# Kernel optimization log

Hardware: AMD Instinct MI355X
Metric: run time of the kernel (lower is better)

## Reference

```python
import jax, jax.numpy as jnp
import numpy as np

IN_F, OUT_F, NB = 4096, 4096, 8
BS = IN_F // NB  # 512


def setup_inputs() -> dict:
    key = jax.random.key(0)
    k1, k2, k3, k4 = jax.random.split(key, 4)
    weight = jax.random.normal(k1, (OUT_F, IN_F), dtype=jnp.float32) * 0.02
    bias = jax.random.normal(k2, (OUT_F,), dtype=jnp.float32) * 0.02
    x = jax.random.normal(k3, (4, 2048, IN_F), dtype=jnp.float32)
    R_blocks = jax.random.normal(k4, (NB, BS, BS), dtype=jnp.float32) * 0.1
    return {"weight": weight, "bias": bias, "x": x, "R_blocks": R_blocks, "layer_idx": 0}


def cayley_transform(A):
    # A: [nb, bs, bs]; Q = (I - A_skew) @ inv(I + A_skew + 1e-6 I)
    bs = A.shape[-1]
    I = jnp.eye(bs, dtype=A.dtype)
    A_skew = 0.5 * (A - jnp.swapaxes(A, -2, -1))
    return jnp.matmul(I - A_skew, jnp.linalg.inv(I + A_skew + 1e-6 * I))


def reference(weight, bias, x, R_blocks, layer_idx):
    R_ortho = cayley_transform(R_blocks)  # [nb, bs, bs]
    # weight @ block_diag(R) == per-block contraction on the in_features axis
    w = weight.reshape(OUT_F, NB, BS)
    tw = jnp.einsum('onb,nbc->onc', w, R_ortho).reshape(OUT_F, IN_F)
    # F.linear: x @ tw.T + bias
    out = jnp.einsum('bsi,oi->bso', x, tw) + bias
    return out
```

## Files before the change

### kernel.cpp

```cpp
#include <hip/hip_runtime.h>
#include <hip/hip_bf16.h>


typedef unsigned short u16;
typedef __attribute__((ext_vector_type(8))) __bf16 bf16x8;
typedef __attribute__((ext_vector_type(4))) float f32x4;
typedef __attribute__((ext_vector_type(8))) unsigned short u16x8;
typedef __attribute__((ext_vector_type(4))) unsigned short u16x4;

#define C0   1.000001f
#define C1Q  2.000001f
#define AS1 __attribute__((address_space(1)))
#define AS3 __attribute__((address_space(3)))

__device__ __forceinline__ u16 f2bf(float x) {
  union { float f; unsigned u; } v; v.f = x;
  return (u16)((v.u + 0x7fffu + ((v.u >> 16) & 1u)) >> 16);
}
__device__ __forceinline__ float bf2f(u16 h) {
  union { float f; unsigned u; } v; v.u = ((unsigned)h) << 16; return v.f;
}

__global__ __launch_bounds__(256) void k_build_M(const float* __restrict__ R,
                                                 u16* __restrict__ Mh,
                                                 u16* __restrict__ Ml) {
  __shared__ float t1[32][33];
  const int n = blockIdx.z;
  const int tr = blockIdx.y * 32, tc = blockIdx.x * 32;
  const int ly = threadIdx.x >> 5, lx = threadIdx.x & 31;
  const float* Rb = R + (size_t)n * 262144;
  float a[4];
#pragma unroll
  for (int i = 0; i < 4; ++i) {
    a[i] = Rb[(size_t)(tr + ly + i * 8) * 512 + tc + lx];
    t1[ly + i * 8][lx] = Rb[(size_t)(tc + ly + i * 8) * 512 + tr + lx];
  }
  __syncthreads();
#pragma unroll
  for (int i = 0; i < 4; ++i) {
    const int r = tr + ly + i * 8, c = tc + lx;
    float m = 0.5f * (a[i] - t1[lx][ly + i * 8]) + (r == c ? C0 : 0.0f);
    u16 h = f2bf(m);
    const size_t idx = (size_t)n * 262144 + (size_t)r * 512 + c;
    Mh[idx] = h;
    Ml[idx] = f2bf(m - bf2f(h));
  }
}

__global__ __launch_bounds__(1024) void k_frob_alpha(const u16* __restrict__ G4,
                                                     float* __restrict__ alpha) {
  __shared__ float red[16];
  const int n = blockIdx.x, tid = threadIdx.x;
  const u16* src = G4 + (size_t)n * 262144;
  float s = 0.f;
  for (int i = tid; i < 32768; i += 1024) {
    u16x8 v = reinterpret_cast<const u16x8*>(src)[i];
#pragma unroll
    for (int e = 0; e < 8; ++e) { float f = bf2f(v[e]); s += f * f; }
  }
  for (int off = 32; off; off >>= 1) s += __shfl_down(s, off, 64);
  if ((tid & 63) == 0) red[tid >> 6] = s;
  __syncthreads();
  if (tid == 0) {
    float t = 0.f;
    for (int q = 0; q < 16; ++q) t += red[q];
    float lam = powf(t, 0.125f);
    alpha[n] = 2.0f / (C0 * C0 + lam);
  }
}

__global__ __launch_bounds__(256) void k_init_X0(const u16* __restrict__ Mh,
                                                 const u16* __restrict__ Ml,
                                                 const float* __restrict__ alpha,
                                                 u16* __restrict__ X0,
                                                 u16* __restrict__ X0t) {
  int idx = blockIdx.x * 256 + threadIdx.x;
  int n = idx >> 18, r = (idx >> 9) & 511, c = idx & 511;
  float m = bf2f(Mh[idx]) + bf2f(Ml[idx]);
  float a = alpha[n];
  X0[idx]  = f2bf(a * ((r == c ? 2.0f * C0 : 0.0f) - m));
  X0t[idx] = f2bf(a * m);
}

template <int PROD3, int DMODE, int OMODE>
__global__ __launch_bounds__(256)
void k_bmm(const u16* __restrict__ Ah, const u16* __restrict__ Al,
           const u16* __restrict__ Bh, const u16* __restrict__ Bl,
           const u16* __restrict__ Dh, const u16* __restrict__ Dl,
           u16* __restrict__ Cnh, u16* __restrict__ Cnl,
           u16* __restrict__ Cth, u16* __restrict__ Ctl,
           float* __restrict__ Cf, float cd, float cs) {
  __shared__ __align__(16) u16 sAh[2048], sBh[2048];
  __shared__ __align__(16) u16 sAl[PROD3 ? 2048 : 8], sBl[PROD3 ? 2048 : 8];
  const size_t zb = (size_t)blockIdx.z * 262144;
  const int tid = threadIdx.x, lane = tid & 63, wave = tid >> 6;
  const int m0 = blockIdx.y * 64, n0 = blockIdx.x * 64;
  const int wr = wave >> 1, wc = wave & 1;
  const int c15 = lane & 15, lk = lane >> 4;
  const int srow = tid >> 2;
  const int sg = (tid & 3) ^ (srow & 3);
  f32x4 acc[2][2] = {};
  const u16* pa = Ah + zb + (size_t)(m0 + srow) * 512 + sg * 8;
  const u16* pb = Bh + zb + (size_t)(n0 + srow) * 512 + sg * 8;

  for (int k0 = 0; k0 < 512; k0 += 32) {
    __builtin_amdgcn_global_load_lds((const AS1 void*)(pa + k0),
                                     (AS3 void*)(sAh + (size_t)tid * 8), 16, 0, 0);
    __builtin_amdgcn_global_load_lds((const AS1 void*)(pb + k0),
                                     (AS3 void*)(sBh + (size_t)tid * 8), 16, 0, 0);
    if constexpr (PROD3) {
      const u16* pal = Al + zb + (size_t)(m0 + srow) * 512 + sg * 8;
      const u16* pbl = Bl + zb + (size_t)(n0 + srow) * 512 + sg * 8;
      __builtin_amdgcn_global_load_lds((const AS1 void*)(pal + k0),
                                       (AS3 void*)(sAl + (size_t)tid * 8), 16, 0, 0);
      __builtin_amdgcn_global_load_lds((const AS1 void*)(pbl + k0),
                                       (AS3 void*)(sBl + (size_t)tid * 8), 16, 0, 0);
    }
    __syncthreads();
    bf16x8 a[2], b[2], al2[2], bl2[2];
#pragma unroll
    for (int i = 0; i < 2; ++i) {
      const int fr = wr * 32 + i * 16 + c15;
      const int ia = fr * 32 + ((lk ^ (fr & 3)) * 8);
      a[i] = *reinterpret_cast<const bf16x8*>(&sAh[ia]);
      if constexpr (PROD3) al2[i] = *reinterpret_cast<const bf16x8*>(&sAl[ia]);
    }
#pragma unroll
    for (int j = 0; j < 2; ++j) {
      const int fc = wc * 32 + j * 16 + c15;
      const int ib = fc * 32 + ((lk ^ (fc & 3)) * 8);
      b[j] = *reinterpret_cast<const bf16x8*>(&sBh[ib]);
      if constexpr (PROD3) bl2[j] = *reinterpret_cast<const bf16x8*>(&sBl[ib]);
    }
#pragma unroll
    for (int i = 0; i < 2; ++i)
#pragma unroll
      for (int j = 0; j < 2; ++j) {
        acc[i][j] = __builtin_amdgcn_mfma_f32_16x16x32_bf16(a[i], b[j], acc[i][j], 0, 0, 0);
        if constexpr (PROD3) {
          acc[i][j] = __builtin_amdgcn_mfma_f32_16x16x32_bf16(a[i],   bl2[j], acc[i][j], 0, 0, 0);
          acc[i][j] = __builtin_amdgcn_mfma_f32_16x16x32_bf16(al2[i], b[j],   acc[i][j], 0, 0, 0);
        }
      }
    __syncthreads();
  }
#pragma unroll
  for (int i = 0; i < 2; ++i)
#pragma unroll
    for (int j = 0; j < 2; ++j) {
      const int rowb = m0 + wr * 32 + i * 16 + lk * 4;
      const int col  = n0 + wc * 32 + j * 16 + c15;
      u16 hv[4], lv[4];
#pragma unroll
      for (int r = 0; r < 4; ++r) {
        float val = cs * acc[i][j][r];
        if constexpr (DMODE >= 1) {
          float d = bf2f(Dh[zb + (size_t)(rowb + r) * 512 + col]);
          if constexpr (DMODE == 2) d += bf2f(Dl[zb + (size_t)(rowb + r) * 512 + col]);
          val += cd * d;
        }
        if constexpr (OMODE & 16) Cf[zb + (size_t)(rowb + r) * 512 + col] = val;
        u16 h = f2bf(val);
        if constexpr (OMODE & 1) Cnh[zb + (size_t)(rowb + r) * 512 + col] = h;
        u16 l = 0;
        if constexpr (OMODE & 10) l = f2bf(val - bf2f(h));
        if constexpr (OMODE & 2) Cnl[zb + (size_t)(rowb + r) * 512 + col] = l;
        hv[r] = h; lv[r] = l;
      }
      if constexpr (OMODE & 4) {
        u16x4 v; v[0] = hv[0]; v[1] = hv[1]; v[2] = hv[2]; v[3] = hv[3];
        *reinterpret_cast<u16x4*>(&Cth[zb + (size_t)col * 512 + rowb]) = v;
      }
      if constexpr (OMODE & 8) {
        u16x4 v; v[0] = lv[0]; v[1] = lv[1]; v[2] = lv[2]; v[3] = lv[3];
        *reinterpret_cast<u16x4*>(&Ctl[zb + (size_t)col * 512 + rowb]) = v;
      }
    }
}

template <int SPLIT, int BF16OUT>
__global__ __launch_bounds__(256)
void k_smm(const float* __restrict__ A, int lda, long long astride,
           const float* __restrict__ B, int ldb, long long bstride,
           void* __restrict__ Cv, int ldc, long long cstride,
           const float* __restrict__ D, int ldd, long long dstride,
           float c1, float sgn, int K) {
  __shared__ __align__(16) u16 lA  [128 * 40];
  __shared__ __align__(16) u16 lBT [128 * 40];
  const int nz = blockIdx.z;
  const float* Ab = A + (size_t)nz * astride;
  const float* Bb = B + (size_t)nz * bstride;
  const float* Db = D + (size_t)nz * dstride;
  const int tid = threadIdx.x, lane = tid & 63, wave = tid >> 6;
  const int m0 = blockIdx.y * 128, n0 = blockIdx.x * 128;
  const int wr = wave >> 1, wc = wave & 1;
  f32x4 acc[4][4] = {};

  for (int k0 = 0; k0 < K; k0 += 32) {
    if (k0) __syncthreads();
    {
      const int row = tid >> 1, ks = (tid & 1) * 16;
      const float* src = Ab + (size_t)(m0 + row) * lda + k0 + ks;
      float fv[16];
#pragma unroll
      for (int q = 0; q < 4; ++q) {
        float4 f = *(reinterpret_cast<const float4*>(src) + q);
        fv[q * 4 + 0] = f.x; fv[q * 4 + 1] = f.y; fv[q * 4 + 2] = f.z; fv[q * 4 + 3] = f.w;
      }
      u16x8 w0, w1;
#pragma unroll
      for (int e = 0; e < 8; ++e) { w0[e] = f2bf(fv[e]); w1[e] = f2bf(fv[e + 8]); }
      *reinterpret_cast<u16x8*>(&lA[row * 40 + ks])     = w0;
      *reinterpret_cast<u16x8*>(&lA[row * 40 + ks + 8]) = w1;
    }
    {
      const int kk = tid >> 3, nb = (tid & 7) * 16;
      const float* src = Bb + (size_t)(k0 + kk) * ldb + n0 + nb;
      float fv[16];
#pragma unroll
      for (int q = 0; q < 4; ++q) {
        float4 f = *(reinterpret_cast<const float4*>(src) + q);
        fv[q * 4 + 0] = f.x; fv[q * 4 + 1] = f.y; fv[q * 4 + 2] = f.z; fv[q * 4 + 3] = f.w;
      }
#pragma unroll
      for (int e = 0; e < 16; ++e) lBT[(nb + e) * 40 + kk] = f2bf(fv[e]);
    }
    __syncthreads();
    const int ks = (lane >> 4) * 8;
    bf16x8 af[4], bfr[4];
#pragma unroll
    for (int f = 0; f < 4; ++f) {
      const int ar = wr * 64 + f * 16 + (lane & 15);
      const int bc = wc * 64 + f * 16 + (lane & 15);
      af[f]  = *reinterpret_cast<const bf16x8*>(&lA [ar * 40 + ks]);
      bfr[f] = *reinterpret_cast<const bf16x8*>(&lBT[bc * 40 + ks]);
    }
#pragma unroll
    for (int i = 0; i < 4; ++i)
#pragma unroll
      for (int j = 0; j < 4; ++j)
        acc[i][j] = __builtin_amdgcn_mfma_f32_16x16x32_bf16(af[i], bfr[j], acc[i][j], 0, 0, 0);
  }
#pragma unroll
  for (int i = 0; i < 4; ++i) {
    const int rowb = m0 + wr * 64 + i * 16 + ((lane >> 4) << 2);
#pragma unroll
    for (int j = 0; j < 4; ++j) {
      const int col = n0 + wc * 64 + j * 16 + (lane & 15);
#pragma unroll
      for (int r = 0; r < 4; ++r) {
        float val = sgn * acc[i][j][r];
        if (c1 != 0.0f) val += c1 * Db[(size_t)(rowb + r) * ldd + col];
        if constexpr (BF16OUT)
          reinterpret_cast<u16*>(Cv)[(size_t)nz * cstride + (size_t)(rowb + r) * ldc + col] = f2bf(val);
        else
          reinterpret_cast<float*>(Cv)[(size_t)nz * cstride + (size_t)(rowb + r) * ldc + col] = val;
      }
    }
  }
}

__global__ __launch_bounds__(256) void k_f32_to_bf16(const float* __restrict__ in,
                                                     u16* __restrict__ out) {
  int idx = blockIdx.x * 256 + threadIdx.x;
  const float* src = in + (size_t)idx * 8;
  float4 f0 = *reinterpret_cast<const float4*>(src);
  float4 f1 = *reinterpret_cast<const float4*>(src + 4);
  u16x8 w;
  w[0] = f2bf(f0.x); w[1] = f2bf(f0.y); w[2] = f2bf(f0.z); w[3] = f2bf(f0.w);
  w[4] = f2bf(f1.x); w[5] = f2bf(f1.y); w[6] = f2bf(f1.z); w[7] = f2bf(f1.w);
  *reinterpret_cast<u16x8*>(out + (size_t)idx * 8) = w;
}

#define NSLOT 9

#define PHASE(KH, MH, WM)                                                      \
  {                                                                            \
    const int gsk = gs0 ^ ((KH) ? 4 : 0);                                      \
    if ((MH) == 0) {                                                           \
      _Pragma("unroll")                                                        \
      for (int n = 0; n < 4; ++n)                                              \
        bf[n] = *reinterpret_cast<const bf16x8*>(                              \
            &lds[bslot * 8192 + (bro + n * 16) * 64 + gsk * 8]);               \
    }                                                                          \
    _Pragma("unroll")                                                          \
    for (int m = 0; m < 4; ++m)                                                \
      af[m] = *reinterpret_cast<const bf16x8*>(                                \
          &lds[aslot * 8192 + ((MH) * 64 + m * 16 + c15) * 64 + gsk * 8]);     \
    STAGE();                                                                   \
    __builtin_amdgcn_s_barrier();                                              \
    asm volatile("s_waitcnt lgkmcnt(0)" ::: "memory");                         \
    __builtin_amdgcn_sched_barrier(0);                                         \
    __builtin_amdgcn_s_setprio(1);                                             \
    _Pragma("unroll")                                                          \
    for (int m = 0; m < 4; ++m)                                                \
      _Pragma("unroll")                                                        \
      for (int n = 0; n < 4; ++n)                                              \
        acc[(MH) * 4 + m][n] = __builtin_amdgcn_mfma_f32_16x16x32_bf16(        \
            af[m], bf[n], acc[(MH) * 4 + m][n], 0, 0, 0);                      \
    __builtin_amdgcn_s_setprio(0);                                             \
    __builtin_amdgcn_sched_barrier(0);                                         \
    if ((WM) == 1) asm volatile("s_waitcnt vmcnt(2)" ::: "memory");            \
    if ((WM) == 2) asm volatile("s_waitcnt vmcnt(0)" ::: "memory");            \
    __builtin_amdgcn_s_barrier();                                              \
  }

#define ADV()                                                                  \
  aslot += 4; if (aslot >= NSLOT) aslot -= NSLOT;                              \
  bslot += 4; if (bslot >= NSLOT) bslot -= NSLOT;

__global__ __launch_bounds__(512, 2)
void k_gemm256(const u16* __restrict__ A, const u16* __restrict__ B,
               const float* __restrict__ bias,
               float* __restrict__ C, int N, int K) {
  __shared__ __align__(16) u16 lds[NSLOT * 8192];
  const int tid = threadIdx.x, lane = tid & 63, wave = tid >> 6;
  int bid = blockIdx.y * gridDim.x + blockIdx.x;
  const int cpx = (gridDim.x * gridDim.y) >> 3;
  bid = (bid & 7) * cpx + (bid >> 3);
  const int nbx = N >> 8;
  const int bx = bid % nbx, by = bid / nbx;
  const int m0 = by << 8, n0 = bx << 8;
  const int wr = wave >> 2, wc = wave & 3;
  const int srow = tid >> 3;
  const int scg  = (tid & 7) ^ (srow & 7);
  const int c15 = lane & 15, lq = lane >> 4;
  const int gs0 = lq ^ (lane & 7);
  const int bro = (wc & 1) * 64 + c15;
  const int NT = K >> 6;

  f32x4 acc[8][4] = {};
  bf16x8 af[4], bf[4];

  int jn = 0, jslot = 0;
  auto STAGE = [&]() {
    if (jn < 4 * NT) {
      const int tau_s = jn >> 2, qh = jn & 3;
      const u16* srcb = (qh < 2)
          ? A + (size_t)(m0 + (qh & 1) * 128 + srow) * (size_t)K
          : B + (size_t)(n0 + (qh & 1) * 128 + srow) * (size_t)K;
      const u16* src = srcb + (tau_s << 6) + scg * 8;
      u16* dst = (u16*)lds + jslot * 8192 + wave * 512;
      __builtin_amdgcn_global_load_lds(
          (const AS1 void*)src, (AS3 void*)dst, 16, 0, 0);
      __builtin_amdgcn_global_load_lds(
          (const AS1 void*)(src + (size_t)64 * K), (AS3 void*)(dst + 4096), 16, 0, 0);
    }
    ++jn; jslot = (jslot == NSLOT - 1) ? 0 : jslot + 1;
  };

  STAGE(); STAGE(); STAGE(); STAGE(); STAGE();
  asm volatile("s_waitcnt vmcnt(2)" ::: "memory");
  __builtin_amdgcn_sched_barrier(0);
  __builtin_amdgcn_s_barrier();

  int aslot = wr, bslot = 2 + (wc >> 1);
  for (int tau = 0; tau < NT - 2; ++tau) {
    PHASE(0, 0, 0)
    PHASE(0, 1, 0)
    PHASE(1, 0, 0)
    PHASE(1, 1, 1)
    ADV()
  }
  PHASE(0, 0, 0)
  PHASE(0, 1, 0)
  PHASE(1, 0, 0)
  PHASE(1, 1, 2)
  ADV()
  PHASE(0, 0, 0)
  PHASE(0, 1, 0)
  PHASE(1, 0, 0)
  PHASE(1, 1, 0)

#pragma unroll
  for (int n = 0; n < 4; ++n) {
    const int col = n0 + wc * 64 + n * 16 + c15;
    const float bv = bias[col];
#pragma unroll
    for (int mi = 0; mi < 8; ++mi) {
      const int rowb = m0 + wr * 128 + mi * 16 + (lq << 2);
#pragma unroll
      for (int r = 0; r < 4; ++r)
        C[(size_t)(rowb + r) * N + col] = acc[mi][n][r] + bv;
    }
  }
}

extern "C" void kernel_launch(void* const* d_in, const int* in_sizes, int n_in,
                              void* d_out, int out_size, void* d_ws, size_t ws_size,
                              hipStream_t stream) {
  const float* W    = (const float*)d_in[0];
  const float* bias = (const float*)d_in[1];
  const float* x    = (const float*)d_in[2];
  const float* R    = (const float*)d_in[3];
  float* out = (float*)d_out;

  char* ws = (char*)d_ws;
  u16* x_bf = (u16*)(ws);
  u16* tw   = (u16*)(ws + 67108864);

  char* arena = (char*)d_out;
  auto slot = [&](int i) -> u16* { return (u16*)(arena + (size_t)i * 4194304); };
  u16 *Mh = slot(0), *Ml = slot(1);
  u16 *G = slot(2), *G2 = slot(3), *G4 = slot(4);
  u16 *Xa = slot(5), *Xat = slot(6), *Xb = slot(7), *Xbt = slot(8);
  u16 *Xbl = slot(9), *Xbtl = slot(10);
  u16 *Tt = slot(2);
  u16 *Tth = slot(3), *Ttl = slot(4);
  u16 *X6h = slot(5), *X6l = slot(6);
  u16 *X6th = slot(11), *X6tl = slot(12);
  float* Qf = (float*)(arena + (size_t)13 * 4194304);
  float* alpha = (float*)(arena + (size_t)15 * 4194304);

  const long long BS2 = 262144;
  const dim3 g8(8, 8, 8);
  const u16* NUL = nullptr;

  k_build_M<<<dim3(16, 16, 8), 256, 0, stream>>>(R, Mh, Ml);
  k_bmm<0, 0, 1><<<g8, 256, 0, stream>>>(Mh, NUL, Mh, NUL, NUL, NUL,
                                         G, nullptr, nullptr, nullptr, nullptr, 0.f, 1.f);
  k_bmm<0, 0, 1><<<g8, 256, 0, stream>>>(G, NUL, G, NUL, NUL, NUL,
                                         G2, nullptr, nullptr, nullptr, nullptr, 0.f, 1.f);
  k_bmm<0, 0, 1><<<g8, 256, 0, stream>>>(G2, NUL, G2, NUL, NUL, NUL,
                                         G4, nullptr, nullptr, nullptr, nullptr, 0.f, 1.f);
  k_frob_alpha<<<8, 1024, 0, stream>>>(G4, alpha);
  k_init_X0<<<8192, 256, 0, stream>>>(Mh, Ml, alpha, Xa, Xat);

  u16 *cur = Xa, *curt = Xat, *nxt = Xb, *nxtt = Xbt;
  for (int it = 0; it < 4; ++it) {
    k_bmm<0, 0, 4><<<g8, 256, 0, stream>>>(Mh, NUL, curt, NUL, NUL, NUL,
                                           nullptr, nullptr, Tt, nullptr, nullptr, 0.f, 1.f);
    k_bmm<0, 1, 5><<<g8, 256, 0, stream>>>(cur, NUL, Tt, NUL, cur, NUL,
                                           nxt, nullptr, nxtt, nullptr, nullptr, 2.f, -1.f);
    u16* t;
    t = cur; cur = nxt; nxt = t;
    t = curt; curt = nxtt; nxtt = t;
  }
  k_bmm<0, 0, 4><<<g8, 256, 0, stream>>>(Mh, NUL, curt, NUL, NUL, NUL,
                                         nullptr, nullptr, Tt, nullptr, nullptr, 0.f, 1.f);
  k_bmm<0, 1, 15><<<g8, 256, 0, stream>>>(cur, NUL, Tt, NUL, cur, NUL,
                                          Xb, Xbl, Xbt, Xbtl, nullptr, 2.f, -1.f);
  k_bmm<1, 0, 12><<<g8, 256, 0, stream>>>(Mh, Ml, Xbt, Xbtl, NUL, NUL,
                                          nullptr, nullptr, Tth, Ttl, nullptr, 0.f, 1.f);
  k_bmm<1, 2, 15><<<g8, 256, 0, stream>>>(Xb, Xbl, Tth, Ttl, Xb, Xbl,
                                          X6h, X6l, X6th, X6tl, nullptr, 2.f, -1.f);
  k_bmm<1, 2, 16><<<g8, 256, 0, stream>>>(Mh, Ml, X6th, X6tl, X6h, X6l,
                                          nullptr, nullptr, nullptr, nullptr, Qf, C1Q, -1.f);
  k_smm<0, 1><<<dim3(4, 32, 8), 256, 0, stream>>>(W, 4096, 512, Qf, 512, BS2,
                                                  tw, 4096, 512, W, 4096, 512, 0.f, 1.f, 512);
  k_f32_to_bf16<<<16384, 256, 0, stream>>>(x, x_bf);
  k_gemm256<<<dim3(16, 32), 512, 0, stream>>>(x_bf, tw, bias, out, 4096, 4096);
}
```

Baseline: 573.0 us.

## Double-buffer LDS fragment reads to overlap them with MFMA in GEMM

Restructures the GEMM inner loop so each phase's LDS reads for the next sub-tile (A and B fragments) are issued before the current MFMA batch, using ping-pong register buffers. This removes the lgkmcnt(0) wait before every MFMA group and hides LDS latency behind compute. The prologue issues one more stage ahead. It costs more VGPRs for the duplicated fragments, which may pressure the 2-waves-per-SIMD occupancy target, and it adds a subtle stage/slot synchronisation that must still be correct without explicit lgkm waits.

```diff
diff --git a/kernel.cpp b/kernel.cpp
--- a/kernel.cpp
+++ b/kernel.cpp
@@ -274,35 +274,62 @@
 
 #define NSLOT 9
 
-#define PHASE(KH, MH, WM)                                                      \
-  {                                                                            \
-    const int gsk = gs0 ^ ((KH) ? 4 : 0);                                      \
-    if ((MH) == 0) {                                                           \
-      _Pragma("unroll")                                                        \
-      for (int n = 0; n < 4; ++n)                                              \
-        bf[n] = *reinterpret_cast<const bf16x8*>(                              \
-            &lds[bslot * 8192 + (bro + n * 16) * 64 + gsk * 8]);               \
-    }                                                                          \
+#define RD_B(dst, G)                                                           \
+  _Pragma("unroll")                                                            \
+  for (int n = 0; n < 4; ++n)                                                  \
+    dst[n] = *reinterpret_cast<const bf16x8*>(                                 \
+        &lds[bslot * 8192 + (bro + n * 16) * 64 + (G) * 8]);
+
+#define RD_A(dst, MH, G)                                                       \
+  _Pragma("unroll")                                                            \
+  for (int m = 0; m < 4; ++m)                                                  \
+    dst[m] = *reinterpret_cast<const bf16x8*>(                                 \
+        &lds[aslot * 8192 + ((MH) * 64 + m * 16 + c15) * 64 + (G) * 8]);
+
+#define MFMA16(afX, bfX, MH)                                                   \
+  __builtin_amdgcn_s_setprio(1);                                               \
+  _Pragma("unroll")                                                            \
+  for (int m = 0; m < 4; ++m)                                                  \
     _Pragma("unroll")                                                          \
-    for (int m = 0; m < 4; ++m)                                                \
-      af[m] = *reinterpret_cast<const bf16x8*>(                                \
-          &lds[aslot * 8192 + ((MH) * 64 + m * 16 + c15) * 64 + gsk * 8]);     \
+    for (int n = 0; n < 4; ++n)                                                \
+      acc[(MH) * 4 + m][n] = __builtin_amdgcn_mfma_f32_16x16x32_bf16(          \
+          afX[m], bfX[n], acc[(MH) * 4 + m][n], 0, 0, 0);                      \
+  __builtin_amdgcn_s_setprio(0);                                               \
+  __builtin_amdgcn_sched_barrier(0);
+
+#define SBAR() __builtin_amdgcn_s_barrier();
+#define SCHB() __builtin_amdgcn_sched_barrier(0);
+
+#define TILEBODY(WM, LAST)                                                     \
+  {                              \
     STAGE();                                                                   \
-    __builtin_amdgcn_s_barrier();                                              \
-    asm volatile("s_waitcnt lgkmcnt(0)" ::: "memory");                         \
-    __builtin_amdgcn_sched_barrier(0);                                         \
-    __builtin_amdgcn_s_setprio(1);                                             \
-    _Pragma("unroll")                                                          \
-    for (int m = 0; m < 4; ++m)                                                \
-      _Pragma("unroll")                                                        \
-      for (int n = 0; n < 4; ++n)                                              \
-        acc[(MH) * 4 + m][n] = __builtin_amdgcn_mfma_f32_16x16x32_bf16(        \
-            af[m], bf[n], acc[(MH) * 4 + m][n], 0, 0, 0);                      \
-    __builtin_amdgcn_s_setprio(0);                                             \
-    __builtin_amdgcn_sched_barrier(0);                                         \
-    if ((WM) == 1) asm volatile("s_waitcnt vmcnt(2)" ::: "memory");            \
-    if ((WM) == 2) asm volatile("s_waitcnt vmcnt(0)" ::: "memory");            \
-    __builtin_amdgcn_s_barrier();                                              \
+    RD_A(afB, 1, gsA)                                                          \
+    SCHB()                                                                     \
+    MFMA16(afA, bf0, 0)                                                        \
+    SBAR()                                                                     \
+                             \
+    STAGE();                                                                   \
+    RD_B(bf1, gsB)                                                             \
+    RD_A(afA, 0, gsB)                                                          \
+    SCHB()                                                                     \
+    MFMA16(afB, bf0, 1)                                                        \
+    SBAR()                                                                     \
+                                 \
+    STAGE();                                                                   \
+    RD_A(afB, 1, gsB)                                                          \
+    SCHB()                                                                     \
+    MFMA16(afA, bf1, 0)                                                        \
+    SBAR()                                                                     \
+        \
+    STAGE();                                                                   \
+    if ((WM) == 1) { asm volatile("s_waitcnt vmcnt(2)" ::: "memory"); SCHB() } \
+    if ((WM) == 2) { asm volatile("s_waitcnt vmcnt(0)" ::: "memory"); SCHB() } \
+    SBAR()                                                                     \
+    ADV()                                                                      \
+    if (!(LAST)) { RD_B(bf0, gsA) RD_A(afA, 0, gsA) }                          \
+    SCHB()                                                                     \
+    MFMA16(afB, bf1, 1)                                                        \
+    SBAR()                                                                     \
   }
 
 #define ADV()                                                                  \
@@ -326,11 +353,12 @@
   const int scg  = (tid & 7) ^ (srow & 7);
   const int c15 = lane & 15, lq = lane >> 4;
   const int gs0 = lq ^ (lane & 7);
+  const int gsA = gs0, gsB = gs0 ^ 4;
   const int bro = (wc & 1) * 64 + c15;
   const int NT = K >> 6;
 
   f32x4 acc[8][4] = {};
-  bf16x8 af[4], bf[4];
+  bf16x8 afA[4], afB[4], bf0[4], bf1[4];
 
   int jn = 0, jslot = 0;
   auto STAGE = [&]() {
@@ -349,28 +377,20 @@
     ++jn; jslot = (jslot == NSLOT - 1) ? 0 : jslot + 1;
   };
 
-  STAGE(); STAGE(); STAGE(); STAGE(); STAGE();
-  asm volatile("s_waitcnt vmcnt(2)" ::: "memory");
-  __builtin_amdgcn_sched_barrier(0);
-  __builtin_amdgcn_s_barrier();
-
+  STAGE(); STAGE(); STAGE(); STAGE(); STAGE(); STAGE();
+  asm volatile("s_waitcnt vmcnt(4)" ::: "memory");
+  SCHB()
+  SBAR()
   int aslot = wr, bslot = 2 + (wc >> 1);
+  RD_B(bf0, gsA)
+  RD_A(afA, 0, gsA)
+  SCHB()
+
   for (int tau = 0; tau < NT - 2; ++tau) {
-    PHASE(0, 0, 0)
-    PHASE(0, 1, 0)
-    PHASE(1, 0, 0)
-    PHASE(1, 1, 1)
-    ADV()
-  }
-  PHASE(0, 0, 0)
-  PHASE(0, 1, 0)
-  PHASE(1, 0, 0)
-  PHASE(1, 1, 2)
-  ADV()
-  PHASE(0, 0, 0)
-  PHASE(0, 1, 0)
-  PHASE(1, 0, 0)
-  PHASE(1, 1, 0)
+    TILEBODY(1, 0)
+  }
+  TILEBODY(2, 0)
+  TILEBODY(0, 1)
 
 #pragma unroll
   for (int n = 0; n < 4; ++n) {
```

Measured after the change: 583.2 us. No clear change (+1.8%).
